# Kernel tuning notes

Measured on AMD Instinct MI355X. Metric: run time of the kernel, lower is better.

Reference implementation:

```python
import jax, jax.numpy as jnp
import numpy as np

N = 50000
E = 800000
D_IN = 256
HID = 64
HEADS = 4
OUT = 86
EPS_BN = 1e-5
NEG_SLOPE = 0.2


def setup_inputs() -> dict:
    key = jax.random.key(0)
    ks = jax.random.split(key, 16)
    HC = HEADS * HID
    inp = {
        "x": jax.random.normal(ks[0], (N, D_IN), jnp.float32),
        "edge_index": jax.random.randint(ks[1], (2, E), 0, N, jnp.int64),
        # GATConv 1: in=D_IN, out per head=HID, concat=True
        "W1": jax.random.normal(ks[2], (D_IN, HC), jnp.float32) * (1.0 / np.sqrt(D_IN)),
        "att_src1": jax.random.normal(ks[3], (HEADS, HID), jnp.float32) * 0.1,
        "att_dst1": jax.random.normal(ks[4], (HEADS, HID), jnp.float32) * 0.1,
        "b1": jnp.zeros((HC,), jnp.float32),
        # GATConv 2: in=HC, out per head=HID, concat=False (mean over heads)
        "W2": jax.random.normal(ks[5], (HC, HC), jnp.float32) * (1.0 / np.sqrt(HC)),
        "att_src2": jax.random.normal(ks[6], (HEADS, HID), jnp.float32) * 0.1,
        "att_dst2": jax.random.normal(ks[7], (HEADS, HID), jnp.float32) * 0.1,
        "b2": jnp.zeros((HID,), jnp.float32),
        # BatchNorms
        "g1": jnp.ones((HC,), jnp.float32),
        "be1": jnp.zeros((HC,), jnp.float32),
        "g2": jnp.ones((HID,), jnp.float32),
        "be2": jnp.zeros((HID,), jnp.float32),
        # PReLU (single shared weight, torch default init 0.25)
        "prelu_w": jnp.asarray(0.25, jnp.float32),
        # final Linear
        "fcW": jax.random.normal(ks[8], (HID, OUT), jnp.float32) * (1.0 / np.sqrt(HID)),
        "fcb": jnp.zeros((OUT,), jnp.float32),
    }
    return inp


def _gat_conv(x, src, dst, W, att_src, att_dst, bias, concat):
    # PyG GATConv forward (dropout inactive in eval mode).
    n = x.shape[0]
    H, C = att_src.shape
    h = (x @ W).reshape(n, H, C)                      # [N,H,C]
    a_s = jnp.sum(h * att_src[None], axis=-1)         # [N,H]
    a_d = jnp.sum(h * att_dst[None], axis=-1)         # [N,H]
    logits = jax.nn.leaky_relu(a_s[src] + a_d[dst], NEG_SLOPE)  # [E,H]
    # segment softmax over edges grouped by destination node
    m = jax.ops.segment_max(logits, dst, num_segments=n)        # [N,H]
    e = jnp.exp(logits - m[dst])
    s = jax.ops.segment_sum(e, dst, num_segments=n)             # [N,H]
    alpha = e / (s[dst] + 1e-16)                                # [E,H]
    msg = h[src] * alpha[:, :, None]                            # [E,H,C]
    out = jax.ops.segment_sum(msg, dst, num_segments=n)         # [N,H,C]
    if concat:
        return out.reshape(n, H * C) + bias
    return out.mean(axis=1) + bias


def _batch_norm(x, gamma, beta):
    mu = x.mean(axis=0)
    var = x.var(axis=0)
    return gamma * (x - mu) * jax.lax.rsqrt(var + EPS_BN) + beta


def reference(x, edge_index, W1, att_src1, att_dst1, b1, W2, att_src2, att_dst2, b2,
              g1, be1, g2, be2, prelu_w, fcW, fcb):
    n = x.shape[0]
    # GATConv default add_self_loops=True
    loops = jnp.arange(n, dtype=edge_index.dtype)
    src = jnp.concatenate([edge_index[0], loops])
    dst = jnp.concatenate([edge_index[1], loops])

    h = _gat_conv(x, src, dst, W1, att_src1, att_dst1, b1, concat=True)
    h = _batch_norm(h, g1, be1)
    h = jnp.where(h >= 0, h, prelu_w * h)             # PReLU
    # dropout: identity (eval)
    h = _gat_conv(h, src, dst, W2, att_src2, att_dst2, b2, concat=False)
    h = _batch_norm(h, g2, be2)
    h = jax.nn.elu(h)
    return h @ fcW + fcb
```

## Files before the change

kernel.cpp:

```cpp
#include <hip/hip_runtime.h>
#include <math.h>

#define LEAKY 0.2f
#define NBMAX 256

typedef __attribute__((ext_vector_type(8))) short short8;
typedef __attribute__((ext_vector_type(4))) float f32x4;

__device__ __forceinline__ float leaky02(float z) { return z >= 0.f ? z : LEAKY * z; }
__device__ __forceinline__ unsigned short f2bf(float f) {
  unsigned u = __float_as_uint(f);
  unsigned r = u + 0x7fffu + ((u >> 16) & 1u);
  return (unsigned short)(r >> 16);
}
__device__ __forceinline__ float bflo(unsigned u) { return __uint_as_float(u << 16); }
__device__ __forceinline__ float bfhi(unsigned u) { return __uint_as_float(u & 0xffff0000u); }


__global__ __launch_bounds__(256) void bktcount_kernel(const int* __restrict__ ei,
                                                       int* __restrict__ bucketCnt,
                                                       int E, int N, int NB) {
  __shared__ int bc[NBMAX];
  for (int i = threadIdx.x; i < NB; i += 256) bc[i] = 0;
  __syncthreads();
  int EP = E + N;
  int chunk = (EP + gridDim.x - 1) / gridDim.x;
  int lo = blockIdx.x * chunk, hi = min(EP, lo + chunk);
  for (int e = lo + threadIdx.x; e < hi; e += 256) {
    int d = (e < E) ? ei[E + e] : (e - E);
    atomicAdd(&bc[d >> 8], 1);
  }
  __syncthreads();
  for (int i = threadIdx.x; i < NB; i += 256)
    if (bc[i]) atomicAdd(&bucketCnt[i], bc[i]);
}

__global__ __launch_bounds__(256) void bktscan_kernel(const int* __restrict__ bucketCnt,
                                                      int* __restrict__ bucketOff,
                                                      int* __restrict__ bucketCur, int NB) {
  int tid = threadIdx.x;
  int lane = tid & 63, wv = tid >> 6;
  int v = (tid < NB) ? bucketCnt[tid] : 0;
  int x = v;
#pragma unroll
  for (int off = 1; off < 64; off <<= 1) {
    int t = __shfl_up(x, off);
    if (lane >= off) x += t;
  }
  __shared__ int ws[4];
  if (lane == 63) ws[wv] = x;
  __syncthreads();
  int woff = 0;
#pragma unroll
  for (int w = 0; w < 4; ++w) if (w < wv) woff += ws[w];
  int incl = x + woff;
  if (tid < NB) {
    bucketOff[tid] = incl - v;
    bucketCur[tid] = incl - v;
  }
  if (tid == NB - 1) bucketOff[NB] = incl;
}

__global__ __launch_bounds__(256) void bktscatter_kernel(const int* __restrict__ ei,
                                                         int* __restrict__ bucketCur,
                                                         unsigned* __restrict__ pairs,
                                                         int E, int N, int NB) {
  __shared__ int bc[NBMAX];
  __shared__ int bbase[NBMAX];
  for (int i = threadIdx.x; i < NB; i += 256) bc[i] = 0;
  __syncthreads();
  int EP = E + N;
  int chunk = (EP + gridDim.x - 1) / gridDim.x;
  int lo = blockIdx.x * chunk, hi = min(EP, lo + chunk);
  for (int e = lo + threadIdx.x; e < hi; e += 256) {
    int d = (e < E) ? ei[E + e] : (e - E);
    atomicAdd(&bc[d >> 8], 1);
  }
  __syncthreads();
  for (int i = threadIdx.x; i < NB; i += 256) {
    int c = bc[i];
    bbase[i] = c ? atomicAdd(&bucketCur[i], c) : 0;
    bc[i] = 0;
  }
  __syncthreads();
  for (int e = lo + threadIdx.x; e < hi; e += 256) {
    int s, d;
    if (e < E) { s = ei[e]; d = ei[E + e]; } else { s = e - E; d = s; }
    int b = d >> 8;
    int slot = bbase[b] + atomicAdd(&bc[b], 1);
    pairs[slot] = ((unsigned)s << 8) | (unsigned)(d & 255);
  }
}

__global__ __launch_bounds__(256) void bktcsr_kernel(const unsigned* __restrict__ pairs,
                                                     const int* __restrict__ bucketOff,
                                                     int* __restrict__ rowptr,
                                                     int* __restrict__ srcs, int N, int NB) {
  int b = blockIdx.x;
  int tid = threadIdx.x;
  __shared__ int cnt[256], loff[256], cur[256];
  cnt[tid] = 0;
  cur[tid] = 0;
  __syncthreads();
  int p0 = bucketOff[b], p1 = bucketOff[b + 1];
  for (int j = p0 + tid; j < p1; j += 256)
    atomicAdd(&cnt[pairs[j] & 255], 1);
  __syncthreads();
  int v = cnt[tid];
  int lane = tid & 63, wv = tid >> 6;
  int x = v;
#pragma unroll
  for (int off = 1; off < 64; off <<= 1) {
    int t = __shfl_up(x, off);
    if (lane >= off) x += t;
  }
  __shared__ int ws[4];
  if (lane == 63) ws[wv] = x;
  __syncthreads();
  int woff = 0;
#pragma unroll
  for (int w = 0; w < 4; ++w) if (w < wv) woff += ws[w];
  int excl = x + woff - v;
  loff[tid] = excl;
  int node = (b << 8) + tid;
  if (node < N) rowptr[node] = p0 + excl;
  if (b == NB - 1 && tid == 255) rowptr[N] = p1;
  __syncthreads();
  for (int j = p0 + tid; j < p1; j += 256) {
    unsigned pr = pairs[j];
    int ln = pr & 255;
    int slot = p0 + loff[ln] + atomicAdd(&cur[ln], 1);
    srcs[slot] = pr >> 8;
  }
}

__global__ void convw_kernel(const float* __restrict__ W1, const float* __restrict__ W2,
                             unsigned short* __restrict__ Wt1, unsigned short* __restrict__ Wt2) {
  int idx = blockIdx.x * 256 + threadIdx.x;
  const float* W;
  unsigned short* Wt;
  if (idx < 65536) { W = W1; Wt = Wt1; } else { W = W2; Wt = Wt2; idx -= 65536; }
  int c = idx >> 8, k = idx & 255;
  Wt[c * 256 + k] = f2bf(W[k * 256 + c]);
}

template <bool BF16A>
__global__ __launch_bounds__(512) void gemm_kernel(const void* __restrict__ Av,
                                                   const unsigned short* __restrict__ Wt,
                                                   unsigned short* __restrict__ Hout, int M,
                                                   const float* __restrict__ bnsc,
                                                   const float* __restrict__ bnsh,
                                                   const float* __restrict__ pwp,
                                                   const float* __restrict__ att_s,
                                                   const float* __restrict__ att_d,
                                                   float* __restrict__ as_o,
                                                   float* __restrict__ ad_o) {
  __shared__ unsigned short As[128][40];
  __shared__ unsigned short Bs[256][40];
  int tid = threadIdx.x;
  int bm = blockIdx.x * 128;
  int l = tid & 63, wv = tid >> 6;
  int wm = wv >> 2, wn = wv & 3;
  int lr = l & 15, lk = l >> 4;
  f32x4 acc[4][4] = {};
  bool hasbn = (bnsc != nullptr);
  float pws = pwp ? pwp[0] : 0.f;

  for (int k0 = 0; k0 < 256; k0 += 32) {
    {
      int row = tid >> 2, kq = (tid & 3) * 8;
      int gr = bm + row;
      if (BF16A) {
        uint4 u = make_uint4(0, 0, 0, 0);
        if (gr < M) u = *(const uint4*)((const unsigned short*)Av + (size_t)gr * 256 + k0 + kq);
        if (hasbn) {
          float4 sc0 = *(const float4*)&bnsc[k0 + kq];
          float4 sh0 = *(const float4*)&bnsh[k0 + kq];
          float4 sc1 = *(const float4*)&bnsc[k0 + kq + 4];
          float4 sh1 = *(const float4*)&bnsh[k0 + kq + 4];
          float v0 = fmaf(bflo(u.x), sc0.x, sh0.x);
          float v1 = fmaf(bfhi(u.x), sc0.y, sh0.y);
          float v2 = fmaf(bflo(u.y), sc0.z, sh0.z);
          float v3 = fmaf(bfhi(u.y), sc0.w, sh0.w);
          float v4 = fmaf(bflo(u.z), sc1.x, sh1.x);
          float v5 = fmaf(bfhi(u.z), sc1.y, sh1.y);
          float v6 = fmaf(bflo(u.w), sc1.z, sh1.z);
          float v7 = fmaf(bfhi(u.w), sc1.w, sh1.w);
          v0 = v0 >= 0.f ? v0 : v0 * pws; v1 = v1 >= 0.f ? v1 : v1 * pws;
          v2 = v2 >= 0.f ? v2 : v2 * pws; v3 = v3 >= 0.f ? v3 : v3 * pws;
          v4 = v4 >= 0.f ? v4 : v4 * pws; v5 = v5 >= 0.f ? v5 : v5 * pws;
          v6 = v6 >= 0.f ? v6 : v6 * pws; v7 = v7 >= 0.f ? v7 : v7 * pws;
          ushort4 o0, o1;
          o0.x = f2bf(v0); o0.y = f2bf(v1); o0.z = f2bf(v2); o0.w = f2bf(v3);
          o1.x = f2bf(v4); o1.y = f2bf(v5); o1.z = f2bf(v6); o1.w = f2bf(v7);
          *(ushort4*)&As[row][kq] = o0;
          *(ushort4*)&As[row][kq + 4] = o1;
        } else {
          *(uint4*)&As[row][kq] = u;
        }
      } else {
        float4 a0 = make_float4(0.f, 0.f, 0.f, 0.f), a1 = a0;
        if (gr < M) {
          a0 = *(const float4*)((const float*)Av + (size_t)gr * 256 + k0 + kq);
          a1 = *(const float4*)((const float*)Av + (size_t)gr * 256 + k0 + kq + 4);
        }
        ushort4 o0, o1;
        o0.x = f2bf(a0.x); o0.y = f2bf(a0.y); o0.z = f2bf(a0.z); o0.w = f2bf(a0.w);
        o1.x = f2bf(a1.x); o1.y = f2bf(a1.y); o1.z = f2bf(a1.z); o1.w = f2bf(a1.w);
        *(ushort4*)&As[row][kq] = o0;
        *(ushort4*)&As[row][kq + 4] = o1;
      }
    }
#pragma unroll
    for (int it = 0; it < 2; ++it) {
      int i = tid + it * 512;
      int c = i >> 2, kq = (i & 3) * 8;
      *(uint4*)&Bs[c][kq] = *(const uint4*)&Wt[(size_t)c * 256 + k0 + kq];
    }
    __syncthreads();
    short8 af[4], bfr[4];
#pragma unroll
    for (int mt = 0; mt < 4; ++mt) af[mt] = *(const short8*)&As[wm * 64 + mt * 16 + lr][lk * 8];
#pragma unroll
    for (int nt = 0; nt < 4; ++nt) bfr[nt] = *(const short8*)&Bs[wn * 64 + nt * 16 + lr][lk * 8];
#pragma unroll
    for (int mt = 0; mt < 4; ++mt)
#pragma unroll
      for (int nt = 0; nt < 4; ++nt)
        acc[mt][nt] = __builtin_amdgcn_mfma_f32_16x16x32_bf16(af[mt], bfr[nt], acc[mt][nt], 0, 0, 0);
    __syncthreads();
  }
  float asv[4], adv[4];
#pragma unroll
  for (int nt = 0; nt < 4; ++nt) {
    int gc = wn * 64 + nt * 16 + lr;
    asv[nt] = att_s[gc];
    adv[nt] = att_d[gc];
  }
#pragma unroll
  for (int mt = 0; mt < 4; ++mt) {
#pragma unroll
    for (int r = 0; r < 4; ++r) {
      int gr = bm + wm * 64 + mt * 16 + lk * 4 + r;
      float ps = acc[mt][0][r] * asv[0] + acc[mt][1][r] * asv[1] +
                 acc[mt][2][r] * asv[2] + acc[mt][3][r] * asv[3];
      float pd = acc[mt][0][r] * adv[0] + acc[mt][1][r] * adv[1] +
                 acc[mt][2][r] * adv[2] + acc[mt][3][r] * adv[3];
#pragma unroll
      for (int off = 1; off < 16; off <<= 1) {
        ps += __shfl_xor(ps, off);
        pd += __shfl_xor(pd, off);
      }
      if (lr == 0 && gr < M) {
        as_o[gr * 4 + wn] = ps;
        ad_o[gr * 4 + wn] = pd;
      }
      if (gr < M) {
#pragma unroll
        for (int nt = 0; nt < 4; ++nt)
          Hout[(size_t)gr * 256 + wn * 64 + nt * 16 + lr] = f2bf(acc[mt][nt][r]);
      }
    }
  }
}

__global__ __launch_bounds__(256) void agg_kernel(const unsigned short* __restrict__ h,
                                                  const float* __restrict__ as_,
                                                  const float* __restrict__ ad_,
                                                  const int* __restrict__ rowptr,
                                                  const int* __restrict__ srcs,
                                                  const float* __restrict__ bias,
                                                  unsigned short* __restrict__ out_bf,
                                                  float* __restrict__ out_f,
                                                  int N, int concat) {
  int l = threadIdx.x & 63;
  int n = blockIdx.x * 4 + (threadIdx.x >> 6);
  if (n >= N) return;
  int e0 = rowptr[n], e1 = rowptr[n + 1];
  int deg = e1 - e0;
  int hh = l >> 4, le = l & 15;
  float adh = ad_[n * 4 + hh];

  if (deg <= 64) {
    int sidx[4];
    float lg[4];
#pragma unroll
    for (int t = 0; t < 4; ++t) {
      int j = e0 + le + 16 * t;
      if (j < e1) {
        int s = srcs[j];
        sidx[t] = s;
        lg[t] = leaky02(as_[s * 4 + hh] + adh);
      } else {
        sidx[t] = 0;
        lg[t] = -1e30f;
      }
    }
    float mx = fmaxf(fmaxf(lg[0], lg[1]), fmaxf(lg[2], lg[3]));
#pragma unroll
    for (int off = 1; off < 16; off <<= 1) mx = fmaxf(mx, __shfl_xor(mx, off));
    float ex[4];
    float sm = 0.f;
#pragma unroll
    for (int t = 0; t < 4; ++t) {
      ex[t] = (lg[t] > -1e29f) ? __expf(lg[t] - mx) : 0.f;
      sm += ex[t];
    }
#pragma unroll
    for (int off = 1; off < 16; off <<= 1) sm += __shfl_xor(sm, off);
    float inv = 1.f / (sm + 1e-16f);

    int p = l >> 5, m = l & 31;
    int hb = m >> 3;
    float invb = __shfl(inv, hb << 4);
    float a[8] = {0.f, 0.f, 0.f, 0.f, 0.f, 0.f, 0.f, 0.f};
#pragma unroll
    for (int t = 0; t < 4; ++t) {
      int base = e0 + 16 * t;
      if (base >= e1) break;
      int cntc = min(16, e1 - base);
      int npr = (cntc + 1) >> 1;
      for (int pr = 0; pr < npr; ++pr) {
        int q = 2 * pr + p;
        int s = __shfl(sidx[t], q);
        float al = __shfl(ex[t], q + (hb << 4)) * invb;
        uint4 hv = *(const uint4*)&h[(size_t)s * 256 + m * 8];
        a[0] = fmaf(bflo(hv.x), al, a[0]);
        a[1] = fmaf(bfhi(hv.x), al, a[1]);
        a[2] = fmaf(bflo(hv.y), al, a[2]);
        a[3] = fmaf(bfhi(hv.y), al, a[3]);
        a[4] = fmaf(bflo(hv.z), al, a[4]);
        a[5] = fmaf(bfhi(hv.z), al, a[5]);
        a[6] = fmaf(bflo(hv.w), al, a[6]);
        a[7] = fmaf(bfhi(hv.w), al, a[7]);
      }
    }
#pragma unroll
    for (int i = 0; i < 8; ++i) a[i] += __shfl_xor(a[i], 32);
    if (concat) {
      if (l < 32) {
        float4 b0 = *(const float4*)&bias[m * 8];
        float4 b1 = *(const float4*)&bias[m * 8 + 4];
        ushort4 o0, o1;
        o0.x = f2bf(a[0] + b0.x); o0.y = f2bf(a[1] + b0.y);
        o0.z = f2bf(a[2] + b0.z); o0.w = f2bf(a[3] + b0.w);
        o1.x = f2bf(a[4] + b1.x); o1.y = f2bf(a[5] + b1.y);
        o1.z = f2bf(a[6] + b1.z); o1.w = f2bf(a[7] + b1.w);
        *(ushort4*)&out_bf[(size_t)n * 256 + m * 8] = o0;
        *(ushort4*)&out_bf[(size_t)n * 256 + m * 8 + 4] = o1;
      }
    } else {
#pragma unroll
      for (int i = 0; i < 8; ++i) {
        a[i] += __shfl_xor(a[i], 8);
        a[i] += __shfl_xor(a[i], 16);
      }
      if (l < 8) {
        float4 b0 = *(const float4*)&bias[m * 8];
        float4 b1 = *(const float4*)&bias[m * 8 + 4];
        float4 o0 = make_float4(0.25f * a[0] + b0.x, 0.25f * a[1] + b0.y,
                                0.25f * a[2] + b0.z, 0.25f * a[3] + b0.w);
        float4 o1 = make_float4(0.25f * a[4] + b1.x, 0.25f * a[5] + b1.y,
                                0.25f * a[6] + b1.z, 0.25f * a[7] + b1.w);
        *(float4*)&out_f[(size_t)n * 64 + m * 8] = o0;
        *(float4*)&out_f[(size_t)n * 64 + m * 8 + 4] = o1;
      }
    }
  } else {
    float ad4[4] = {ad_[n * 4], ad_[n * 4 + 1], ad_[n * 4 + 2], ad_[n * 4 + 3]};
    float mx[4] = {-1e30f, -1e30f, -1e30f, -1e30f};
    for (int j = e0 + l; j < e1; j += 64) {
      int s = srcs[j];
      float4 av = *(const float4*)&as_[s * 4];
      mx[0] = fmaxf(mx[0], leaky02(av.x + ad4[0]));
      mx[1] = fmaxf(mx[1], leaky02(av.y + ad4[1]));
      mx[2] = fmaxf(mx[2], leaky02(av.z + ad4[2]));
      mx[3] = fmaxf(mx[3], leaky02(av.w + ad4[3]));
    }
#pragma unroll
    for (int off = 32; off; off >>= 1) {
      mx[0] = fmaxf(mx[0], __shfl_xor(mx[0], off));
      mx[1] = fmaxf(mx[1], __shfl_xor(mx[1], off));
      mx[2] = fmaxf(mx[2], __shfl_xor(mx[2], off));
      mx[3] = fmaxf(mx[3], __shfl_xor(mx[3], off));
    }
    float sm[4] = {0.f, 0.f, 0.f, 0.f};
    for (int j = e0 + l; j < e1; j += 64) {
      int s = srcs[j];
      float4 av = *(const float4*)&as_[s * 4];
      sm[0] += __expf(leaky02(av.x + ad4[0]) - mx[0]);
      sm[1] += __expf(leaky02(av.y + ad4[1]) - mx[1]);
      sm[2] += __expf(leaky02(av.z + ad4[2]) - mx[2]);
      sm[3] += __expf(leaky02(av.w + ad4[3]) - mx[3]);
    }
#pragma unroll
    for (int off = 32; off; off >>= 1) {
      sm[0] += __shfl_xor(sm[0], off);
      sm[1] += __shfl_xor(sm[1], off);
      sm[2] += __shfl_xor(sm[2], off);
      sm[3] += __shfl_xor(sm[3], off);
    }
    float mh = hh == 0 ? mx[0] : hh == 1 ? mx[1] : hh == 2 ? mx[2] : mx[3];
    float sh = hh == 0 ? sm[0] : hh == 1 ? sm[1] : hh == 2 ? sm[2] : sm[3];
    float inv = 1.f / (sh + 1e-16f);
    float a0 = 0.f, a1 = 0.f, a2 = 0.f, a3 = 0.f;
    for (int j = e0; j < e1; ++j) {
      int s = srcs[j];
      float al = __expf(leaky02(as_[s * 4 + hh] + adh) - mh) * inv;
      uint2 hv = *(const uint2*)&h[(size_t)s * 256 + l * 4];
      a0 = fmaf(bflo(hv.x), al, a0); a1 = fmaf(bfhi(hv.x), al, a1);
      a2 = fmaf(bflo(hv.y), al, a2); a3 = fmaf(bfhi(hv.y), al, a3);
    }
    if (concat) {
      float4 b4 = *(const float4*)&bias[l * 4];
      ushort4 o;
      o.x = f2bf(a0 + b4.x); o.y = f2bf(a1 + b4.y);
      o.z = f2bf(a2 + b4.z); o.w = f2bf(a3 + b4.w);
      *(ushort4*)&out_bf[(size_t)n * 256 + l * 4] = o;
    } else {
      a0 += __shfl_xor(a0, 16); a0 += __shfl_xor(a0, 32);
      a1 += __shfl_xor(a1, 16); a1 += __shfl_xor(a1, 32);
      a2 += __shfl_xor(a2, 16); a2 += __shfl_xor(a2, 32);
      a3 += __shfl_xor(a3, 16); a3 += __shfl_xor(a3, 32);
      if (l < 16) {
        float4 b4 = *(const float4*)&bias[l * 4];
        float4 o = make_float4(0.25f * a0 + b4.x, 0.25f * a1 + b4.y,
                               0.25f * a2 + b4.z, 0.25f * a3 + b4.w);
        *(float4*)&out_f[(size_t)n * 64 + l * 4] = o;
      }
    }
  }
}

__global__ __launch_bounds__(256) void bnstats_bf16_kernel(const unsigned short* __restrict__ x,
                                                           float* __restrict__ sum,
                                                           float* __restrict__ ss, int N) {
  int tid = threadIdx.x;
  int c = (tid & 127) * 2;
  int r = blockIdx.x * 2 + (tid >> 7);
  int stride = gridDim.x * 2;
  float a0 = 0.f, b0 = 0.f, a1 = 0.f, b1 = 0.f;
  for (; r < N; r += stride) {
    unsigned u = *(const unsigned*)&x[(size_t)r * 256 + c];
    float v0 = bflo(u), v1 = bfhi(u);
    a0 += v0; b0 += v0 * v0;
    a1 += v1; b1 += v1 * v1;
  }
  atomicAdd(&sum[c], a0); atomicAdd(&ss[c], b0);
  atomicAdd(&sum[c + 1], a1); atomicAdd(&ss[c + 1], b1);
}

__global__ __launch_bounds__(256) void bnstats_kernel(const float* __restrict__ x,
                                                      float* __restrict__ sum, float* __restrict__ ss,
                                                      int N, int C) {
  int tid = threadIdx.x;
  int f = tid % C;
  int rpb = 256 / C;
  int r = blockIdx.x * rpb + tid / C;
  int stride = gridDim.x * rpb;
  float a = 0.f, b = 0.f;
  for (; r < N; r += stride) {
    float v = x[(size_t)r * C + f];
    a += v;
    b += v * v;
  }
  atomicAdd(&sum[f], a);
  atomicAdd(&ss[f], b);
}

__global__ void bnfinalize_kernel(const float* __restrict__ sum, const float* __restrict__ ss,
                                  const float* __restrict__ gamma, const float* __restrict__ beta,
                                  float* __restrict__ scale, float* __restrict__ shift, int N, int C) {
  int f = threadIdx.x;
  if (f >= C) return;
  float mu = sum[f] / (float)N;
  float var = ss[f] / (float)N - mu * mu;
  float sc = gamma[f] * rsqrtf(var + 1e-5f);
  scale[f] = sc;
  shift[f] = beta[f] - mu * sc;
}

__global__ __launch_bounds__(256) void fc_kernel(const float* __restrict__ x,
                                                 const float* __restrict__ sc, const float* __restrict__ sh,
                                                 const float* __restrict__ W, const float* __restrict__ b,
                                                 float* __restrict__ out, int N) {
  __shared__ float ws[64 * 86];
  __shared__ float xs[32 * 64];
  int tid = threadIdx.x;
  for (int i = tid; i < 64 * 86; i += 256) ws[i] = W[i];
  int n0 = blockIdx.x * 32;
  for (int i = tid; i < 32 * 64; i += 256) {
    int n = n0 + (i >> 6), c = i & 63;
    float v = (n < N) ? x[(size_t)n * 64 + c] : 0.f;
    v = fmaf(v, sc[c], sh[c]);
    xs[i] = v > 0.f ? v : expm1f(v);
  }
  __syncthreads();
  for (int idx = tid; idx < 32 * 86; idx += 256) {
    int nl = idx / 86, o = idx % 86;
    int n = n0 + nl;
    if (n >= N) continue;
    float acc = b[o];
    const float* xr = &xs[nl * 64];
#pragma unroll 8
    for (int k = 0; k < 64; ++k) acc = fmaf(xr[k], ws[k * 86 + o], acc);
    out[(size_t)n * 86 + o] = acc;
  }
}

extern "C" void kernel_launch(void* const* d_in, const int* in_sizes, int n_in,
                              void* d_out, int out_size, void* d_ws, size_t ws_size,
                              hipStream_t stream) {
  const float* x    = (const float*)d_in[0];
  const int*   ei   = (const int*)d_in[1];
  const float* W1   = (const float*)d_in[2];
  const float* asw1 = (const float*)d_in[3];
  const float* adw1 = (const float*)d_in[4];
  const float* b1   = (const float*)d_in[5];
  const float* W2   = (const float*)d_in[6];
  const float* asw2 = (const float*)d_in[7];
  const float* adw2 = (const float*)d_in[8];
  const float* b2   = (const float*)d_in[9];
  const float* g1   = (const float*)d_in[10];
  const float* be1  = (const float*)d_in[11];
  const float* g2   = (const float*)d_in[12];
  const float* be2  = (const float*)d_in[13];
  const float* pw   = (const float*)d_in[14];
  const float* fcW  = (const float*)d_in[15];
  const float* fcb  = (const float*)d_in[16];

  const int N = in_sizes[0] / 256;
  const int E = in_sizes[1] / 2;
  const int EP = E + N;
  const int NB = (N + 255) / 256;

  char* ws = (char*)d_ws;
  size_t off = 0;
  auto alloc = [&](size_t bytes) {
    char* p = ws + off;
    off += (bytes + 255) & ~(size_t)255;
    return p;
  };
  unsigned short* h    = (unsigned short*)alloc((size_t)N * 256 * 2);
  unsigned short* outb = (unsigned short*)alloc((size_t)N * 256 * 2);
  float* xm   = (float*)alloc((size_t)N * 64 * 4);
  float* as1  = (float*)alloc((size_t)N * 4 * 4);
  float* ad1  = (float*)alloc((size_t)N * 4 * 4);
  float* as2  = (float*)alloc((size_t)N * 4 * 4);
  float* ad2  = (float*)alloc((size_t)N * 4 * 4);
  int* rowptr = (int*)alloc((size_t)(N + 1) * 4);
  int* srcs   = (int*)alloc((size_t)EP * 4);
  unsigned* pairs = (unsigned*)alloc((size_t)EP * 4);
  int* bucketCnt = (int*)alloc((NBMAX + 1) * 4);
  int* bucketOff = (int*)alloc((NBMAX + 1) * 4);
  int* bucketCur = (int*)alloc((NBMAX + 1) * 4);
  unsigned short* Wt1 = (unsigned short*)alloc(65536 * 2);
  unsigned short* Wt2 = (unsigned short*)alloc(65536 * 2);
  float* bstat = (float*)alloc(512 * 4);
  float* bsum = bstat, *bss = bstat + 256;
  float* bsc  = (float*)alloc(256 * 4);
  float* bsh  = (float*)alloc(256 * 4);
  float* bsc2 = (float*)alloc(64 * 4);
  float* bsh2 = (float*)alloc(64 * 4);

  int ngrid4 = (N + 3) / 4;
  int ggrid = (N + 127) / 128;

  hipMemsetAsync(bucketCnt, 0, (NBMAX + 1) * 4, stream);
  bktcount_kernel<<<256, 256, 0, stream>>>(ei, bucketCnt, E, N, NB);
  convw_kernel<<<512, 256, 0, stream>>>(W1, W2, Wt1, Wt2);
  bktscan_kernel<<<1, 256, 0, stream>>>(bucketCnt, bucketOff, bucketCur, NB);
  bktscatter_kernel<<<256, 256, 0, stream>>>(ei, bucketCur, pairs, E, N, NB);
  bktcsr_kernel<<<NB, 256, 0, stream>>>(pairs, bucketOff, rowptr, srcs, N, NB);

  gemm_kernel<false><<<ggrid, 512, 0, stream>>>(x, Wt1, h, N, nullptr, nullptr, nullptr,
                                                asw1, adw1, as1, ad1);
  agg_kernel<<<ngrid4, 256, 0, stream>>>(h, as1, ad1, rowptr, srcs, b1, outb, nullptr, N, 1);

  hipMemsetAsync(bstat, 0, 512 * 4, stream);
  bnstats_bf16_kernel<<<512, 256, 0, stream>>>(outb, bsum, bss, N);
  bnfinalize_kernel<<<1, 256, 0, stream>>>(bsum, bss, g1, be1, bsc, bsh, N, 256);

  gemm_kernel<true><<<ggrid, 512, 0, stream>>>(outb, Wt2, h, N, bsc, bsh, pw,
                                               asw2, adw2, as2, ad2);
  agg_kernel<<<ngrid4, 256, 0, stream>>>(h, as2, ad2, rowptr, srcs, b2, nullptr, xm, N, 0);

  hipMemsetAsync(bstat, 0, 128 * 4, stream);
  bnstats_kernel<<<512, 256, 0, stream>>>(xm, bstat, bstat + 64, N, 64);
  bnfinalize_kernel<<<1, 64, 0, stream>>>(bstat, bstat + 64, g2, be2, bsc2, bsh2, N, 64);

  fc_kernel<<<(N + 31) / 32, 256, 0, stream>>>(xm, bsc2, bsh2, fcW, fcb, (float*)d_out, N);
}
```

Before: 512.0 us.

## Fuse BN finalize into consumers, compact 16-bit src indices, coalesce GEMM stores, unroll aggregation

Removes both one-block batch-norm finalize kernels by computing scale and shift inside the second GEMM and the FC kernel prologues, which saves launches. It packs source indices as 16-bit values (N=50000 fits) to halve the CSR index traffic. The GEMM output is staged through shared memory so each row is written with 16-byte stores instead of scattered 2-byte ones, at the cost of extra LDS and barriers. The aggregation loop is unrolled by two to keep two gathers in flight. The 16-bit index packing only works for N up to 65535.

```diff
diff --git a/kernel.cpp b/kernel.cpp
--- a/kernel.cpp
+++ b/kernel.cpp
@@ -88,14 +88,15 @@
     if (e < E) { s = ei[e]; d = ei[E + e]; } else { s = e - E; d = s; }
     int b = d >> 8;
     int slot = bbase[b] + atomicAdd(&bc[b], 1);
-    pairs[slot] = ((unsigned)s << 8) | (unsigned)(d & 255);
+    pairs[slot] = ((unsigned)s << 16) | (unsigned)d;
   }
 }
 
 __global__ __launch_bounds__(256) void bktcsr_kernel(const unsigned* __restrict__ pairs,
                                                      const int* __restrict__ bucketOff,
                                                      int* __restrict__ rowptr,
-                                                     int* __restrict__ srcs, int N, int NB) {
+                                                     unsigned short* __restrict__ srcs,
+                                                     int N, int NB) {
   int b = blockIdx.x;
   int tid = threadIdx.x;
   __shared__ int cnt[256], loff[256], cur[256];
@@ -130,7 +131,7 @@
     unsigned pr = pairs[j];
     int ln = pr & 255;
     int slot = p0 + loff[ln] + atomicAdd(&cur[ln], 1);
-    srcs[slot] = pr >> 8;
+    srcs[slot] = (unsigned short)(pr >> 16);
   }
 }
 
@@ -144,12 +145,14 @@
   Wt[c * 256 + k] = f2bf(W[k * 256 + c]);
 }
 
-template <bool BF16A>
+template <bool BF16A, bool HASBN>
 __global__ __launch_bounds__(512) void gemm_kernel(const void* __restrict__ Av,
                                                    const unsigned short* __restrict__ Wt,
                                                    unsigned short* __restrict__ Hout, int M,
-                                                   const float* __restrict__ bnsc,
-                                                   const float* __restrict__ bnsh,
+                                                   const float* __restrict__ bn_sum,
+                                                   const float* __restrict__ bn_ss,
+                                                   const float* __restrict__ gamma,
+                                                   const float* __restrict__ beta,
                                                    const float* __restrict__ pwp,
                                                    const float* __restrict__ att_s,
                                                    const float* __restrict__ att_d,
@@ -157,14 +160,26 @@
                                                    float* __restrict__ ad_o) {
   __shared__ unsigned short As[128][40];
   __shared__ unsigned short Bs[256][40];
+  __shared__ unsigned short stg[8][16][64];
+  __shared__ float bscL[256], bshL[256];
   int tid = threadIdx.x;
   int bm = blockIdx.x * 128;
   int l = tid & 63, wv = tid >> 6;
   int wm = wv >> 2, wn = wv & 3;
   int lr = l & 15, lk = l >> 4;
   f32x4 acc[4][4] = {};
-  bool hasbn = (bnsc != nullptr);
   float pws = pwp ? pwp[0] : 0.f;
+
+  if (HASBN) {
+    for (int i = tid; i < 256; i += 512) {
+      float mu = bn_sum[i] / (float)M;
+      float var = bn_ss[i] / (float)M - mu * mu;
+      float sc = gamma[i] * rsqrtf(var + 1e-5f);
+      bscL[i] = sc;
+      bshL[i] = beta[i] - mu * sc;
+    }
+    __syncthreads();
+  }
 
   for (int k0 = 0; k0 < 256; k0 += 32) {
     {
@@ -173,11 +188,11 @@
       if (BF16A) {
         uint4 u = make_uint4(0, 0, 0, 0);
         if (gr < M) u = *(const uint4*)((const unsigned short*)Av + (size_t)gr * 256 + k0 + kq);
-        if (hasbn) {
-          float4 sc0 = *(const float4*)&bnsc[k0 + kq];
-          float4 sh0 = *(const float4*)&bnsh[k0 + kq];
-          float4 sc1 = *(const float4*)&bnsc[k0 + kq + 4];
-          float4 sh1 = *(const float4*)&bnsh[k0 + kq + 4];
+        if (HASBN) {
+          float4 sc0 = *(const float4*)&bscL[k0 + kq];
+          float4 sh0 = *(const float4*)&bshL[k0 + kq];
+          float4 sc1 = *(const float4*)&bscL[k0 + kq + 4];
+          float4 sh1 = *(const float4*)&bshL[k0 + kq + 4];
           float v0 = fmaf(bflo(u.x), sc0.x, sh0.x);
           float v1 = fmaf(bfhi(u.x), sc0.y, sh0.y);
           float v2 = fmaf(bflo(u.y), sc0.z, sh0.z);
@@ -230,6 +245,7 @@
         acc[mt][nt] = __builtin_amdgcn_mfma_f32_16x16x32_bf16(af[mt], bfr[nt], acc[mt][nt], 0, 0, 0);
     __syncthreads();
   }
+
   float asv[4], adv[4];
 #pragma unroll
   for (int nt = 0; nt < 4; ++nt) {
@@ -255,12 +271,28 @@
         as_o[gr * 4 + wn] = ps;
         ad_o[gr * 4 + wn] = pd;
       }
-      if (gr < M) {
-#pragma unroll
-        for (int nt = 0; nt < 4; ++nt)
-          Hout[(size_t)gr * 256 + wn * 64 + nt * 16 + lr] = f2bf(acc[mt][nt][r]);
-      }
-    }
+    }
+  }
+
+#pragma unroll
+  for (int mt = 0; mt < 4; ++mt) {
+#pragma unroll
+    for (int nt = 0; nt < 4; ++nt)
+#pragma unroll
+      for (int r = 0; r < 4; ++r)
+        stg[wv][lk * 4 + r][nt * 16 + lr] = f2bf(acc[mt][nt][r]);
+    __syncthreads();
+#pragma unroll
+    for (int rd = 0; rd < 2; ++rd) {
+      int idx = tid + rd * 512;
+      int rowslot = idx >> 5, col8 = (idx & 31) * 8;
+      int wm2 = rowslot >> 4, rloc = rowslot & 15;
+      int wn2 = col8 >> 6, c = col8 & 63;
+      int gr = bm + wm2 * 64 + mt * 16 + rloc;
+      if (gr < M)
+        *(uint4*)&Hout[(size_t)gr * 256 + col8] = *(const uint4*)&stg[wm2 * 4 + wn2][rloc][c];
+    }
+    __syncthreads();
   }
 }
 
@@ -268,7 +300,7 @@
                                                   const float* __restrict__ as_,
                                                   const float* __restrict__ ad_,
                                                   const int* __restrict__ rowptr,
-                                                  const int* __restrict__ srcs,
+                                                  const unsigned short* __restrict__ srcs,
                                                   const float* __restrict__ bias,
                                                   unsigned short* __restrict__ out_bf,
                                                   float* __restrict__ out_f,
@@ -311,8 +343,8 @@
     float inv = 1.f / (sm + 1e-16f);
 
     int p = l >> 5, m = l & 31;
-    int hb = m >> 3;
-    float invb = __shfl(inv, hb << 4);
+    int hsel = (m >> 3) << 4;
+    float invb = __shfl(inv, hsel);
     float a[8] = {0.f, 0.f, 0.f, 0.f, 0.f, 0.f, 0.f, 0.f};
 #pragma unroll
     for (int t = 0; t < 4; ++t) {
@@ -320,19 +352,33 @@
       if (base >= e1) break;
       int cntc = min(16, e1 - base);
       int npr = (cntc + 1) >> 1;
-      for (int pr = 0; pr < npr; ++pr) {
+      int pr = 0;
+      for (; pr + 2 <= npr; pr += 2) {
+        int q0 = 2 * pr + p, q1 = q0 + 2;
+        int s0 = __shfl(sidx[t], q0);
+        float al0 = __shfl(ex[t], q0 + hsel) * invb;
+        int s1 = __shfl(sidx[t], q1);
+        float al1 = __shfl(ex[t], q1 + hsel) * invb;
+        uint4 h0 = *(const uint4*)&h[(size_t)s0 * 256 + m * 8];
+        uint4 h1 = *(const uint4*)&h[(size_t)s1 * 256 + m * 8];
+        a[0] = fmaf(bflo(h0.x), al0, a[0]); a[1] = fmaf(bfhi(h0.x), al0, a[1]);
+        a[2] = fmaf(bflo(h0.y), al0, a[2]); a[3] = fmaf(bfhi(h0.y), al0, a[3]);
+        a[4] = fmaf(bflo(h0.z), al0, a[4]); a[5] = fmaf(bfhi(h0.z), al0, a[5]);
+        a[6] = fmaf(bflo(h0.w), al0, a[6]); a[7] = fmaf(bfhi(h0.w), al0, a[7]);
+        a[0] = fmaf(bflo(h1.x), al1, a[0]); a[1] = fmaf(bfhi(h1.x), al1, a[1]);
+        a[2] = fmaf(bflo(h1.y), al1, a[2]); a[3] = fmaf(bfhi(h1.y), al1, a[3]);
+        a[4] = fmaf(bflo(h1.z), al1, a[4]); a[5] = fmaf(bfhi(h1.z), al1, a[5]);
+        a[6] = fmaf(bflo(h1.w), al1, a[6]); a[7] = fmaf(bfhi(h1.w), al1, a[7]);
+      }
+      if (pr < npr) {
         int q = 2 * pr + p;
         int s = __shfl(sidx[t], q);
-        float al = __shfl(ex[t], q + (hb << 4)) * invb;
+        float al = __shfl(ex[t], q + hsel) * invb;
         uint4 hv = *(const uint4*)&h[(size_t)s * 256 + m * 8];
-        a[0] = fmaf(bflo(hv.x), al, a[0]);
-        a[1] = fmaf(bfhi(hv.x), al, a[1]);
-        a[2] = fmaf(bflo(hv.y), al, a[2]);
-        a[3] = fmaf(bfhi(hv.y), al, a[3]);
-        a[4] = fmaf(bflo(hv.z), al, a[4]);
-        a[5] = fmaf(bfhi(hv.z), al, a[5]);
-        a[6] = fmaf(bflo(hv.w), al, a[6]);
-        a[7] = fmaf(bfhi(hv.w), al, a[7]);
+        a[0] = fmaf(bflo(hv.x), al, a[0]); a[1] = fmaf(bfhi(hv.x), al, a[1]);
+        a[2] = fmaf(bflo(hv.y), al, a[2]); a[3] = fmaf(bfhi(hv.y), al, a[3]);
+        a[4] = fmaf(bflo(hv.z), al, a[4]); a[5] = fmaf(bfhi(hv.z), al, a[5]);
+        a[6] = fmaf(bflo(hv.w), al, a[6]); a[7] = fmaf(bfhi(hv.w), al, a[7]);
       }
     }
 #pragma unroll
@@ -468,31 +514,31 @@
   atomicAdd(&ss[f], b);
 }
 
-__global__ void bnfinalize_kernel(const float* __restrict__ sum, const float* __restrict__ ss,
-                                  const float* __restrict__ gamma, const float* __restrict__ beta,
-                                  float* __restrict__ scale, float* __restrict__ shift, int N, int C) {
-  int f = threadIdx.x;
-  if (f >= C) return;
-  float mu = sum[f] / (float)N;
-  float var = ss[f] / (float)N - mu * mu;
-  float sc = gamma[f] * rsqrtf(var + 1e-5f);
-  scale[f] = sc;
-  shift[f] = beta[f] - mu * sc;
-}
-
 __global__ __launch_bounds__(256) void fc_kernel(const float* __restrict__ x,
-                                                 const float* __restrict__ sc, const float* __restrict__ sh,
+                                                 const float* __restrict__ bn_sum,
+                                                 const float* __restrict__ bn_ss,
+                                                 const float* __restrict__ gamma,
+                                                 const float* __restrict__ beta,
                                                  const float* __restrict__ W, const float* __restrict__ b,
                                                  float* __restrict__ out, int N) {
   __shared__ float ws[64 * 86];
   __shared__ float xs[32 * 64];
+  __shared__ float scL[64], shL[64];
   int tid = threadIdx.x;
+  if (tid < 64) {
+    float mu = bn_sum[tid] / (float)N;
+    float var = bn_ss[tid] / (float)N - mu * mu;
+    float sc = gamma[tid] * rsqrtf(var + 1e-5f);
+    scL[tid] = sc;
+    shL[tid] = beta[tid] - mu * sc;
+  }
   for (int i = tid; i < 64 * 86; i += 256) ws[i] = W[i];
+  __syncthreads();
   int n0 = blockIdx.x * 32;
   for (int i = tid; i < 32 * 64; i += 256) {
     int n = n0 + (i >> 6), c = i & 63;
     float v = (n < N) ? x[(size_t)n * 64 + c] : 0.f;
-    v = fmaf(v, sc[c], sh[c]);
+    v = fmaf(v, scL[c], shL[c]);
     xs[i] = v > 0.f ? v : expm1f(v);
   }
   __syncthreads();
@@ -549,7 +595,7 @@
   float* as2  = (float*)alloc((size_t)N * 4 * 4);
   float* ad2  = (float*)alloc((size_t)N * 4 * 4);
   int* rowptr = (int*)alloc((size_t)(N + 1) * 4);
-  int* srcs   = (int*)alloc((size_t)EP * 4);
+  unsigned short* srcs = (unsigned short*)alloc((size_t)EP * 2);
   unsigned* pairs = (unsigned*)alloc((size_t)EP * 4);
   int* bucketCnt = (int*)alloc((NBMAX + 1) * 4);
   int* bucketOff = (int*)alloc((NBMAX + 1) * 4);
@@ -558,10 +604,6 @@
   unsigned short* Wt2 = (unsigned short*)alloc(65536 * 2);
   float* bstat = (float*)alloc(512 * 4);
   float* bsum = bstat, *bss = bstat + 256;
-  float* bsc  = (float*)alloc(256 * 4);
-  float* bsh  = (float*)alloc(256 * 4);
-  float* bsc2 = (float*)alloc(64 * 4);
-  float* bsh2 = (float*)alloc(64 * 4);
 
   int ngrid4 = (N + 3) / 4;
   int ggrid = (N + 127) / 128;
@@ -573,21 +615,22 @@
   bktscatter_kernel<<<256, 256, 0, stream>>>(ei, bucketCur, pairs, E, N, NB);
   bktcsr_kernel<<<NB, 256, 0, stream>>>(pairs, bucketOff, rowptr, srcs, N, NB);
 
-  gemm_kernel<false><<<ggrid, 512, 0, stream>>>(x, Wt1, h, N, nullptr, nullptr, nullptr,
-                                                asw1, adw1, as1, ad1);
+  gemm_kernel<false, false><<<ggrid, 512, 0, stream>>>(x, Wt1, h, N,
+                                                       nullptr, nullptr, nullptr, nullptr, nullptr,
+                                                       asw1, adw1, as1, ad1);
   agg_kernel<<<ngrid4, 256, 0, stream>>>(h, as1, ad1, rowptr, srcs, b1, outb, nullptr, N, 1);
 
   hipMemsetAsync(bstat, 0, 512 * 4, stream);
   bnstats_bf16_kernel<<<512, 256, 0, stream>>>(outb, bsum, bss, N);
-  bnfinalize_kernel<<<1, 256, 0, stream>>>(bsum, bss, g1, be1, bsc, bsh, N, 256);
-
-  gemm_kernel<true><<<ggrid, 512, 0, stream>>>(outb, Wt2, h, N, bsc, bsh, pw,
-                                               asw2, adw2, as2, ad2);
+
+  gemm_kernel<true, true><<<ggrid, 512, 0, stream>>>(outb, Wt2, h, N,
+                                                     bsum, bss, g1, be1, pw,
+                                                     asw2, adw2, as2, ad2);
   agg_kernel<<<ngrid4, 256, 0, stream>>>(h, as2, ad2, rowptr, srcs, b2, nullptr, xm, N, 0);
 
   hipMemsetAsync(bstat, 0, 128 * 4, stream);
   bnstats_kernel<<<512, 256, 0, stream>>>(xm, bstat, bstat + 64, N, 64);
-  bnfinalize_kernel<<<1, 64, 0, stream>>>(bstat, bstat + 64, g2, be2, bsc2, bsh2, N, 64);
-
-  fc_kernel<<<(N + 31) / 32, 256, 0, stream>>>(xm, bsc2, bsh2, fcW, fcb, (float*)d_out, N);
-}
+
+  fc_kernel<<<(N + 31) / 32, 256, 0, stream>>>(xm, bstat, bstat + 64, g2, be2,
+                                               fcW, fcb, (float*)d_out, N);
+}
```

Result: no change. 516.8 us (+0.9%).
